# Performance work log

Measured on AMD Instinct MI355X. Metric: run time of the kernel, lower is better.

Reference implementation:

```python
import jax, jax.numpy as jnp
import numpy as np

V, E, G = 25000, 50000, 1024
D_IN, E_IN, D, EH = 74, 12, 64, 128
STEPS, S2S, L, NT = 6, 6, 3, 1


def setup_inputs() -> dict:
    key = jax.random.key(0)
    ks = jax.random.split(key, 20)
    p = lambda k, shp: (jax.random.normal(k, shp, jnp.float32) * 0.05)
    return {
        "node_feats": jax.random.normal(ks[0], (V, D_IN), jnp.float32),
        "edge_feats": jax.random.normal(ks[1], (E, E_IN), jnp.float32),
        "src": jax.random.randint(ks[2], (E,), 0, V),
        "dst": jax.random.randint(ks[3], (E,), 0, V),
        "node2graph": jnp.sort(jax.random.randint(ks[4], (V,), 0, G)),
        "W_proj": p(ks[5], (D_IN, D)), "b_proj": jnp.zeros((D,), jnp.float32),
        "W_e1": p(ks[6], (E_IN, EH)), "b_e1": jnp.zeros((EH,), jnp.float32),
        "W_e2": p(ks[7], (EH, D * D)), "b_e2": jnp.zeros((D * D,), jnp.float32),
        "b_conv": jnp.zeros((D,), jnp.float32),
        "gru_W_ih": p(ks[8], (3 * D, D)), "gru_W_hh": p(ks[9], (3 * D, D)),
        "gru_b_ih": jnp.zeros((3 * D,), jnp.float32), "gru_b_hh": jnp.zeros((3 * D,), jnp.float32),
        "lstm_W_ih0": p(ks[10], (4 * D, 2 * D)), "lstm_W_hh0": p(ks[11], (4 * D, D)),
        "lstm_b_ih0": jnp.zeros((4 * D,), jnp.float32), "lstm_b_hh0": jnp.zeros((4 * D,), jnp.float32),
        "lstm_W_ih_r": p(ks[12], (L - 1, 4 * D, D)), "lstm_W_hh_r": p(ks[13], (L - 1, 4 * D, D)),
        "lstm_b_ih_r": jnp.zeros((L - 1, 4 * D), jnp.float32), "lstm_b_hh_r": jnp.zeros((L - 1, 4 * D), jnp.float32),
        "W1": p(ks[14], (2 * D, D)), "b1": jnp.zeros((D,), jnp.float32),
        "bn_gamma": jnp.ones((D,), jnp.float32), "bn_beta": jnp.zeros((D,), jnp.float32),
        "bn_mean": jnp.zeros((D,), jnp.float32), "bn_var": jnp.ones((D,), jnp.float32),
        "W2": p(ks[15], (D, 4 * NT)), "b2": jnp.zeros((4 * NT,), jnp.float32),
    }


def reference(node_feats, edge_feats, src, dst, node2graph,
              W_proj, b_proj, W_e1, b_e1, W_e2, b_e2, b_conv,
              gru_W_ih, gru_W_hh, gru_b_ih, gru_b_hh,
              lstm_W_ih0, lstm_W_hh0, lstm_b_ih0, lstm_b_hh0,
              lstm_W_ih_r, lstm_W_hh_r, lstm_b_ih_r, lstm_b_hh_r,
              W1, b1, bn_gamma, bn_beta, bn_mean, bn_var, W2, b2):
    # --- MPNNGNN: project + ReLU, then NNConv(sum) + ReLU + GRU, x STEPS ---
    h = jax.nn.relu(node_feats @ W_proj + b_proj)                       # (V, D)
    # edge network: per-edge (D,D) mixing matrix (edge_feats constant across steps)
    We = (jax.nn.relu(edge_feats @ W_e1 + b_e1) @ W_e2 + b_e2).reshape(E, D, D)

    def mp_step(hh, _):
        m = jnp.einsum('ed,edo->eo', hh[src], We)                       # per-edge message
        agg = jax.ops.segment_sum(m, dst, num_segments=V) + b_conv      # NNConv sum + bias
        x = jax.nn.relu(agg)
        gi = x @ gru_W_ih.T + gru_b_ih                                  # GRU (torch gate order r,z,n)
        gh = hh @ gru_W_hh.T + gru_b_hh
        ir, iz, inn = jnp.split(gi, 3, axis=-1)
        hr, hz, hn = jnp.split(gh, 3, axis=-1)
        r = jax.nn.sigmoid(ir + hr)
        z = jax.nn.sigmoid(iz + hz)
        n = jnp.tanh(inn + r * hn)
        return (1.0 - z) * n + z * hh, None

    h, _ = jax.lax.scan(mp_step, h, None, length=STEPS)

    # --- Set2Set readout ---
    q_star = jnp.zeros((G, 2 * D), h.dtype)
    hs = jnp.zeros((L, G, D), h.dtype)
    cs = jnp.zeros((L, G, D), h.dtype)
    for _ in range(S2S):
        x = q_star
        nh, nc = [], []
        for l in range(L):                                              # stacked LSTM, seq len 1
            Wih = lstm_W_ih0 if l == 0 else lstm_W_ih_r[l - 1]
            Whh = lstm_W_hh0 if l == 0 else lstm_W_hh_r[l - 1]
            bih = lstm_b_ih0 if l == 0 else lstm_b_ih_r[l - 1]
            bhh = lstm_b_hh0 if l == 0 else lstm_b_hh_r[l - 1]
            gates = x @ Wih.T + bih + hs[l] @ Whh.T + bhh               # torch order i,f,g,o
            i, f, g, o = jnp.split(gates, 4, axis=-1)
            c = jax.nn.sigmoid(f) * cs[l] + jax.nn.sigmoid(i) * jnp.tanh(g)
            hc = jax.nn.sigmoid(o) * jnp.tanh(c)
            nh.append(hc); nc.append(c)
            x = hc
        hs, cs = jnp.stack(nh), jnp.stack(nc)
        q = x                                                           # (G, D)
        e = jnp.sum(h * q[node2graph], axis=-1)                         # (V,) attention logits
        emax = jax.lax.stop_gradient(jax.ops.segment_max(e, node2graph, num_segments=G))
        emax = jnp.where(jnp.isfinite(emax), emax, 0.0)
        ez = jnp.exp(e - emax[node2graph])                              # per-graph softmax
        denom = jax.ops.segment_sum(ez, node2graph, num_segments=G)
        alpha = ez / jnp.maximum(denom[node2graph], 1e-12)
        readout = jax.ops.segment_sum(h * alpha[:, None], node2graph, num_segments=G)
        q_star = jnp.concatenate([q, readout], axis=-1)                 # (G, 2D)

    # --- evidential head: Linear + ReLU + BatchNorm(eval) + Linear ---
    h1 = jax.nn.relu(q_star @ W1 + b1)
    hbn = bn_gamma * (h1 - bn_mean) * jax.lax.rsqrt(bn_var + 1e-5) + bn_beta
    out = hbn @ W2 + b2                                                 # (G, 4*NT)
    means, logl, loga, logb = jnp.split(out, 4, axis=1)
    MINV = 1e-6
    lam = jax.nn.softplus(logl) + MINV
    alp = jax.nn.softplus(loga) + MINV + 1.0
    bet = jax.nn.softplus(logb) + MINV
    return jnp.stack([means, lam, alp, bet], axis=2).reshape(out.shape)
```

## Files before the change

### kernel.cpp

```cpp
#include <hip/hip_runtime.h>
#include <stdint.h>

#define V_N 25000
#define E_N 50000
#define G_N 1024
#define DIN 74
#define EIN 12
#define NSTEPS 6
#define NS2S 6
#define MPAD 50048

typedef unsigned int u32;
typedef unsigned short u16;
typedef __attribute__((ext_vector_type(8))) short bf16x8v;
typedef __attribute__((ext_vector_type(4))) float f32x4v;

typedef __attribute__((address_space(3))) void lds_void;
typedef __attribute__((address_space(1))) void gbl_void;

__device__ __forceinline__ void gload_lds16(const void* g, void* l) {
  __builtin_amdgcn_global_load_lds((gbl_void*)g, (lds_void*)l, 16, 0, 0);
}

__device__ __forceinline__ u16 f2bf(float f) {
  u32 u = __float_as_uint(f);
  u = (u + 0x7fffu + ((u >> 16) & 1u)) >> 16;
  return (u16)u;
}
__device__ __forceinline__ u32 pack2bf(float lo, float hi) {
  return (u32)f2bf(lo) | ((u32)f2bf(hi) << 16);
}
__device__ __forceinline__ float bflo(u32 w){ return __uint_as_float(w << 16); }
__device__ __forceinline__ float bfhi(u32 w){ return __uint_as_float(w & 0xffff0000u); }
__device__ __forceinline__ float sigf(float x){ return 1.f/(1.f + expf(-x)); }
__device__ __forceinline__ float splusf(float x){ return fmaxf(x, 0.f) + log1pf(expf(-fabsf(x))); }

__global__ void prep_kernel(const float* gWih, const float* gWhh,
                            const float* lWih0, const float* lWhh0,
                            const float* lWihr, const float* lWhhr,
                            const float* We2,
                            float* gWihT, float* gWhhT,
                            u32* TW40, u32* TU40, u32* TW4r, u32* TU4r,
                            u16* WbT) {
  int idx = blockIdx.x * 256 + threadIdx.x;
  if (idx < 12288) { int d = idx / 192, r = idx % 192; gWihT[idx] = gWih[r*64 + d]; return; }
  idx -= 12288;
  if (idx < 12288) { int d = idx / 192, r = idx % 192; gWhhT[idx] = gWhh[r*64 + d]; return; }
  idx -= 12288;
  if (idx < 16384) { int q = idx >> 2, j = idx & 3; int k8 = q >> 8, r = q & 255;
                     TW40[idx] = pack2bf(lWih0[r*128 + k8*8 + 2*j], lWih0[r*128 + k8*8 + 2*j + 1]); return; }
  idx -= 16384;
  if (idx < 8192)  { int q = idx >> 2, j = idx & 3; int k8 = q >> 8, r = q & 255;
                     TU40[idx] = pack2bf(lWhh0[r*64 + k8*8 + 2*j], lWhh0[r*64 + k8*8 + 2*j + 1]); return; }
  idx -= 8192;
  if (idx < 16384) { int l = idx >> 13, rem = idx & 8191; int q = rem >> 2, j = rem & 3;
                     int k8 = q >> 8, r = q & 255;
                     TW4r[idx] = pack2bf(lWihr[l*16384 + r*64 + k8*8 + 2*j],
                                         lWihr[l*16384 + r*64 + k8*8 + 2*j + 1]); return; }
  idx -= 16384;
  if (idx < 16384) { int l = idx >> 13, rem = idx & 8191; int q = rem >> 2, j = rem & 3;
                     int k8 = q >> 8, r = q & 255;
                     TU4r[idx] = pack2bf(lWhhr[l*16384 + r*64 + k8*8 + 2*j],
                                         lWhhr[l*16384 + r*64 + k8*8 + 2*j + 1]); return; }
  idx -= 16384;
  { int n = idx / 128, k = idx % 128; WbT[idx] = f2bf(We2[k*4096 + n]); }
}

__global__ void proj_kernel(const float* nf, const float* Wp, const float* bp, float* h) {
  int v = blockIdx.x * 4 + (threadIdx.x >> 6);
  int o = threadIdx.x & 63;
  if (v >= V_N) return;
  float acc = bp[o];
  const float* row = nf + (size_t)v * DIN;
  #pragma unroll 2
  for (int d = 0; d < DIN; ++d) acc += row[d] * Wp[d*64 + o];
  h[(size_t)v*64 + o] = fmaxf(acc, 0.f);
}

__global__ void edgenet_kernel(const float* ef, const float* W1, const float* b1, u16* zb) {
  int e = blockIdx.x * 2 + (threadIdx.x >> 7);
  int k = threadIdx.x & 127;
  float acc = 0.f;
  if (e < E_N) {
    acc = b1[k];
    const float* row = ef + (size_t)e * EIN;
    #pragma unroll
    for (int i = 0; i < EIN; ++i) acc += row[i] * W1[i*128 + k];
    acc = fmaxf(acc, 0.f);
  }
  zb[(size_t)e*128 + k] = f2bf(acc);
}

__global__ __launch_bounds__(512) void fusedmsg_kernel(const u16* zb, const u16* WbT, const float* be2,
                                                       const float* h, const int* src, const int* dst,
                                                       float* agg) {
  __shared__ __align__(16) u16 Bs[2][8192];
  __shared__ float hS[128][66];
  int t = threadIdx.x;
  int e0 = blockIdx.x * 128;
  int w = t >> 6, lane = t & 63;
  int l16 = lane & 15, lh = lane >> 4;

  for (int it = 0; it < 16; ++it) {
    int idx = it * 512 + t;
    int el = idx >> 6, d = idx & 63;
    int e = e0 + el;
    int sv = (e < E_N) ? src[e] : 0;
    hS[el][d] = h[(size_t)sv * 64 + d];
  }

  bf16x8v af[4];
  #pragma unroll
  for (int ks = 0; ks < 4; ++ks)
    af[ks] = *(const bf16x8v*)(zb + (size_t)(e0 + w*16 + l16)*128 + ks*32 + lh*8);

  {
    const char* Bg = (const char*)WbT;
    char* Bl = (char*)Bs[0];
    #pragma unroll
    for (int it = 0; it < 2; ++it) {
      int f = it * 512 + t;
      int r = f >> 4, s = f & 15;
      int gc = s ^ (r & 7);
      gload_lds16(Bg + r*256 + gc*16, Bl + (size_t)(f & ~63) * 16);
    }
  }
  __syncthreads();

  float macc[4][4];
  #pragma unroll
  for (int of = 0; of < 4; ++of)
    #pragma unroll
    for (int r = 0; r < 4; ++r) macc[of][r] = 0.f;

  for (int d = 0; d < 64; ++d) {
    int buf = d & 1;
    if (d < 63) {
      const char* Bg = (const char*)WbT + (size_t)(d + 1) * 16384;
      char* Bl = (char*)Bs[buf ^ 1];
      #pragma unroll
      for (int it = 0; it < 2; ++it) {
        int f = it * 512 + t;
        int r = f >> 4, s = f & 15;
        int gc = s ^ (r & 7);
        gload_lds16(Bg + r*256 + gc*16, Bl + (size_t)(f & ~63) * 16);
      }
    }
    float hv[4];
    #pragma unroll
    for (int r = 0; r < 4; ++r) hv[r] = hS[w*16 + lh*4 + r][d];

    const char* Bb = (const char*)Bs[buf];
    #pragma unroll
    for (int of = 0; of < 4; ++of) {
      float bias = be2[d*64 + of*16 + l16];
      f32x4v c = (f32x4v){bias, bias, bias, bias};
      #pragma unroll
      for (int ks = 0; ks < 4; ++ks) {
        int brow = of*16 + l16;
        int cb = ks*4 + lh;
        bf16x8v bf = *(const bf16x8v*)(Bb + brow*256 + ((cb ^ (brow & 7)) << 4));
        c = __builtin_amdgcn_mfma_f32_16x16x32_bf16(af[ks], bf, c, 0, 0, 0);
      }
      #pragma unroll
      for (int r = 0; r < 4; ++r) macc[of][r] += hv[r] * c[r];
    }
    __syncthreads();
  }

  #pragma unroll
  for (int r = 0; r < 4; ++r) {
    int row = w*16 + lh*4 + r;
    int e = e0 + row;
    if (e < E_N) {
      int dv = dst[e];
      #pragma unroll
      for (int of = 0; of < 4; ++of)
        atomicAdd(&agg[(size_t)dv*64 + of*16 + l16], macc[of][r]);
    }
  }
}

__global__ void gru_kernel(const float* aggc, const float* bconv, const float* WihT, const float* WhhT,
                           const float* bih, const float* bhh, float* h, float* aggz) {
  int wbase = (blockIdx.x * 4 + (threadIdx.x >> 6)) * 4;
  int o = threadIdx.x & 63;
  float xv[4], hv[4];
  #pragma unroll
  for (int n = 0; n < 4; ++n) {
    int v = wbase + n;
    if (v < V_N) { xv[n] = fmaxf(aggc[(size_t)v*64 + o] + bconv[o], 0.f); hv[n] = h[(size_t)v*64 + o]; }
    else { xv[n] = 0.f; hv[n] = 0.f; }
  }
  float ar[4] = {0,0,0,0}, az[4] = {0,0,0,0}, an[4] = {0,0,0,0};
  float br[4] = {0,0,0,0}, bz[4] = {0,0,0,0}, bn2[4] = {0,0,0,0};
  #pragma unroll 4
  for (int d = 0; d < 64; ++d) {
    float wr = WihT[d*192 + o], wz = WihT[d*192 + 64 + o], wn = WihT[d*192 + 128 + o];
    float ur = WhhT[d*192 + o], uz = WhhT[d*192 + 64 + o], un = WhhT[d*192 + 128 + o];
    #pragma unroll
    for (int n = 0; n < 4; ++n) {
      float xd = __shfl(xv[n], d);
      float hd = __shfl(hv[n], d);
      ar[n] += xd*wr; az[n] += xd*wz; an[n] += xd*wn;
      br[n] += hd*ur; bz[n] += hd*uz; bn2[n] += hd*un;
    }
  }
  float b_r = bih[o] + bhh[o], b_z = bih[64+o] + bhh[64+o];
  float bin = bih[128+o], bhn = bhh[128+o];
  #pragma unroll
  for (int n = 0; n < 4; ++n) {
    int v = wbase + n;
    if (v >= V_N) continue;
    float r  = sigf(ar[n] + br[n] + b_r);
    float z  = sigf(az[n] + bz[n] + b_z);
    float nn = tanhf(an[n] + bin + r*(bn2[n] + bhn));
    h[(size_t)v*64 + o] = (1.f - z)*nn + z*hv[n];
    aggz[(size_t)v*64 + o] = 0.f;
  }
}

__global__ void gstart_kernel(const int* n2g, int* gstart) {
  int g = blockIdx.x * 256 + threadIdx.x;
  if (g > G_N) return;
  int lo = 0, hi = V_N;
  while (lo < hi) { int mid = (lo + hi) >> 1; if (n2g[mid] < g) lo = mid + 1; else hi = mid; }
  gstart[g] = lo;
}

__global__ __launch_bounds__(256) void s2s_kernel(const float* h, const int* gstart,
    const uint4* TW40, const uint4* TU40, const uint4* TW4r, const uint4* TU4r,
    const float* bih0, const float* bhh0, const float* bihr, const float* bhhr,
    float* qstar) {
  __shared__ float sq[4][128];
  __shared__ float sx[4][128];
  __shared__ float shs[4][3][64], scs[4][3][64];
  __shared__ float sg[4][256];
  int tt = threadIdx.x;
  int g0blk = blockIdx.x * 4;
  int w = tt >> 6, lane = tt & 63;
  int nstart = gstart[g0blk + w], nend = gstart[g0blk + w + 1];

  for (int i = tt; i < 512; i += 256) ((float*)sq)[i] = 0.f;
  for (int i = tt; i < 768; i += 256) { ((float*)shs)[i] = 0.f; ((float*)scs)[i] = 0.f; }
  __syncthreads();

  for (int iter = 0; iter < NS2S; ++iter) {
    for (int i = tt; i < 512; i += 256) ((float*)sx)[i] = ((float*)sq)[i];
    __syncthreads();

    for (int l = 0; l < 3; ++l) {
      const uint4* TW = (l == 0) ? TW40 : TW4r + (size_t)(l-1) * 2048;
      const uint4* TU = (l == 0) ? TU40 : TU4r + (size_t)(l-1) * 2048;
      const float* bi = (l == 0) ? bih0 : bihr + (l-1)*256;
      const float* bh = (l == 0) ? bhh0 : bhhr + (l-1)*256;
      float bsum = bi[tt] + bh[tt];
      float acc[4] = {bsum, bsum, bsum, bsum};
      if (l == 0) {
        #pragma unroll
        for (int k8 = 0; k8 < 16; ++k8) {
          uint4 u = TW[k8*256 + tt];
          #pragma unroll
          for (int gi = 0; gi < 4; ++gi) {
            const float4 xa = *(const float4*)&sx[gi][k8*8];
            const float4 xb = *(const float4*)&sx[gi][k8*8 + 4];
            acc[gi] += xa.x*bflo(u.x) + xa.y*bfhi(u.x) + xa.z*bflo(u.y) + xa.w*bfhi(u.y)
                     + xb.x*bflo(u.z) + xb.y*bfhi(u.z) + xb.z*bflo(u.w) + xb.w*bfhi(u.w);
          }
        }
      } else {
        #pragma unroll
        for (int k8 = 0; k8 < 8; ++k8) {
          uint4 u = TW[k8*256 + tt];
          #pragma unroll
          for (int gi = 0; gi < 4; ++gi) {
            const float4 xa = *(const float4*)&sx[gi][k8*8];
            const float4 xb = *(const float4*)&sx[gi][k8*8 + 4];
            acc[gi] += xa.x*bflo(u.x) + xa.y*bfhi(u.x) + xa.z*bflo(u.y) + xa.w*bfhi(u.y)
                     + xb.x*bflo(u.z) + xb.y*bfhi(u.z) + xb.z*bflo(u.w) + xb.w*bfhi(u.w);
          }
        }
      }
      #pragma unroll
      for (int k8 = 0; k8 < 8; ++k8) {
        uint4 u = TU[k8*256 + tt];
        #pragma unroll
        for (int gi = 0; gi < 4; ++gi) {
          const float4 ha = *(const float4*)&shs[gi][l][k8*8];
          const float4 hb = *(const float4*)&shs[gi][l][k8*8 + 4];
          acc[gi] += ha.x*bflo(u.x) + ha.y*bfhi(u.x) + ha.z*bflo(u.y) + ha.w*bfhi(u.y)
                   + hb.x*bflo(u.z) + hb.y*bfhi(u.z) + hb.z*bflo(u.w) + hb.w*bfhi(u.w);
        }
      }
      #pragma unroll
      for (int gi = 0; gi < 4; ++gi) sg[gi][tt] = acc[gi];
      __syncthreads();
      {
        int gq = tt >> 6, r = tt & 63;
        float gv_i = sg[gq][r], gv_f = sg[gq][64+r], gv_g = sg[gq][128+r], gv_o = sg[gq][192+r];
        float c = sigf(gv_f)*scs[gq][l][r] + sigf(gv_i)*tanhf(gv_g);
        float hc = sigf(gv_o)*tanhf(c);
        scs[gq][l][r] = c; shs[gq][l][r] = hc; sx[gq][r] = hc;
      }
      __syncthreads();
    }

    {
      float q_l = sx[w][lane];
      float lmax = -3.4e38f;
      int i = nstart;
      for (; i + 1 < nend; i += 2) {
        float h0 = h[(size_t)i*64 + lane];
        float h1 = h[(size_t)(i+1)*64 + lane];
        float v0 = h0 * q_l, v1 = h1 * q_l;
        #pragma unroll
        for (int off = 32; off; off >>= 1) { v0 += __shfl_xor(v0, off); v1 += __shfl_xor(v1, off); }
        lmax = fmaxf(lmax, fmaxf(v0, v1));
      }
      if (i < nend) {
        float h0 = h[(size_t)i*64 + lane];
        float v0 = h0 * q_l;
        #pragma unroll
        for (int off = 32; off; off >>= 1) v0 += __shfl_xor(v0, off);
        lmax = fmaxf(lmax, v0);
      }
      float lsum = 0.f, accv = 0.f;
      i = nstart;
      for (; i + 1 < nend; i += 2) {
        float h0 = h[(size_t)i*64 + lane];
        float h1 = h[(size_t)(i+1)*64 + lane];
        float v0 = h0 * q_l, v1 = h1 * q_l;
        #pragma unroll
        for (int off = 32; off; off >>= 1) { v0 += __shfl_xor(v0, off); v1 += __shfl_xor(v1, off); }
        float e0 = expf(v0 - lmax), e1 = expf(v1 - lmax);
        lsum += e0 + e1; accv += e0*h0 + e1*h1;
      }
      if (i < nend) {
        float h0 = h[(size_t)i*64 + lane];
        float v0 = h0 * q_l;
        #pragma unroll
        for (int off = 32; off; off >>= 1) v0 += __shfl_xor(v0, off);
        float e0 = expf(v0 - lmax);
        lsum += e0; accv += e0*h0;
      }
      sq[w][lane] = sx[w][lane];
      sq[w][64 + lane] = accv / fmaxf(lsum, 1e-12f);
    }
    __syncthreads();
  }

  for (int i = tt; i < 512; i += 256) qstar[(size_t)g0blk * 128 + i] = ((float*)sq)[i];
}

__global__ void head_kernel(const float* qstar, const float* W1, const float* b1,
                            const float* gma, const float* gbe, const float* gme, const float* gva,
                            const float* W2, const float* b2, float* out) {
  __shared__ float hb[4][64];
  int wslot = threadIdx.x >> 6;
  int g = blockIdx.x * 4 + wslot;
  int o = threadIdx.x & 63;
  float acc = b1[o];
  const float* q = qstar + (size_t)g * 128;
  #pragma unroll 4
  for (int k = 0; k < 128; ++k) acc += q[k] * W1[k*64 + o];
  acc = fmaxf(acc, 0.f);
  float hbn = gma[o] * (acc - gme[o]) * rsqrtf(gva[o] + 1e-5f) + gbe[o];
  hb[wslot][o] = hbn;
  __syncthreads();
  if (o < 4) {
    float v = b2[o];
    #pragma unroll 8
    for (int k = 0; k < 64; ++k) v += hb[wslot][k] * W2[k*4 + o];
    float res;
    if (o == 0) res = v;
    else { res = splusf(v) + 1e-6f; if (o == 2) res += 1.f; }
    out[(size_t)g*4 + o] = res;
  }
}

extern "C" void kernel_launch(void* const* d_in, const int* in_sizes, int n_in,
                              void* d_out, int out_size, void* d_ws, size_t ws_size,
                              hipStream_t stream) {
  const float* node_feats = (const float*)d_in[0];
  const float* edge_feats = (const float*)d_in[1];
  const int*   src        = (const int*)d_in[2];
  const int*   dst        = (const int*)d_in[3];
  const int*   n2g        = (const int*)d_in[4];
  const float* W_proj = (const float*)d_in[5];
  const float* b_proj = (const float*)d_in[6];
  const float* W_e1   = (const float*)d_in[7];
  const float* b_e1   = (const float*)d_in[8];
  const float* W_e2   = (const float*)d_in[9];
  const float* b_e2   = (const float*)d_in[10];
  const float* b_conv = (const float*)d_in[11];
  const float* gru_W_ih = (const float*)d_in[12];
  const float* gru_W_hh = (const float*)d_in[13];
  const float* gru_b_ih = (const float*)d_in[14];
  const float* gru_b_hh = (const float*)d_in[15];
  const float* lstm_W_ih0 = (const float*)d_in[16];
  const float* lstm_W_hh0 = (const float*)d_in[17];
  const float* lstm_b_ih0 = (const float*)d_in[18];
  const float* lstm_b_hh0 = (const float*)d_in[19];
  const float* lstm_W_ih_r = (const float*)d_in[20];
  const float* lstm_W_hh_r = (const float*)d_in[21];
  const float* lstm_b_ih_r = (const float*)d_in[22];
  const float* lstm_b_hh_r = (const float*)d_in[23];
  const float* W1 = (const float*)d_in[24];
  const float* b1 = (const float*)d_in[25];
  const float* bn_gamma = (const float*)d_in[26];
  const float* bn_beta  = (const float*)d_in[27];
  const float* bn_mean  = (const float*)d_in[28];
  const float* bn_var   = (const float*)d_in[29];
  const float* W2 = (const float*)d_in[30];
  const float* b2 = (const float*)d_in[31];

  char* ws = (char*)d_ws;
  size_t off = 0;
  auto alloc = [&](size_t n) { size_t c = off; off += (n + 255) & ~(size_t)255; return c; };
  u16*   zb     = (u16*)  (ws + alloc((size_t)MPAD * 128 * 2));
  float* h      = (float*)(ws + alloc((size_t)V_N * 64 * 4));
  float* agg    = (float*)(ws + alloc((size_t)V_N * 64 * 4));
  u16*   WbT    = (u16*)  (ws + alloc((size_t)4096 * 128 * 2));
  float* gWihT  = (float*)(ws + alloc(12288 * 4));
  float* gWhhT  = (float*)(ws + alloc(12288 * 4));
  u32*   TW40   = (u32*)  (ws + alloc(16384 * 4));
  u32*   TU40   = (u32*)  (ws + alloc(8192 * 4));
  u32*   TW4r   = (u32*)  (ws + alloc(16384 * 4));
  u32*   TU4r   = (u32*)  (ws + alloc(16384 * 4));
  int*   gstart = (int*)  (ws + alloc(1025 * 4));
  float* qstar  = (float*)(ws + alloc((size_t)G_N * 128 * 4));
  (void)in_sizes; (void)n_in; (void)out_size; (void)ws_size;

  prep_kernel<<<2368, 256, 0, stream>>>(gru_W_ih, gru_W_hh, lstm_W_ih0, lstm_W_hh0,
                                        lstm_W_ih_r, lstm_W_hh_r, W_e2,
                                        gWihT, gWhhT, TW40, TU40, TW4r, TU4r, WbT);
  proj_kernel<<<6250, 256, 0, stream>>>(node_feats, W_proj, b_proj, h);
  edgenet_kernel<<<MPAD / 2, 256, 0, stream>>>(edge_feats, W_e1, b_e1, zb);
  hipMemsetAsync(agg, 0, (size_t)V_N * 64 * 4, stream);

  for (int st = 0; st < NSTEPS; ++st) {
    fusedmsg_kernel<<<MPAD / 128, 512, 0, stream>>>(zb, WbT, b_e2, h, src, dst, agg);
    gru_kernel<<<1563, 256, 0, stream>>>(agg, b_conv, gWihT, gWhhT, gru_b_ih, gru_b_hh, h, agg);
  }

  gstart_kernel<<<5, 256, 0, stream>>>(n2g, gstart);
  s2s_kernel<<<256, 256, 0, stream>>>(h, gstart, (const uint4*)TW40, (const uint4*)TU40,
                                      (const uint4*)TW4r, (const uint4*)TU4r,
                                      lstm_b_ih0, lstm_b_hh0, lstm_b_ih_r, lstm_b_hh_r, qstar);
  head_kernel<<<256, 256, 0, stream>>>(qstar, W1, b1, bn_gamma, bn_beta, bn_mean, bn_var,
                                       W2, b2, (float*)d_out);
}
```

Baseline: 1.081 ms.

## Split message kernel over input-dim halves with 2 row fragments per wave

The fused NNConv message kernel now runs two blocks per 128-edge tile, each covering half of the 64 input dimensions, with 256 threads where each wave handles 32 edges (two MFMA row fragments) so every B fragment loaded from LDS feeds two MFMAs. Gathered source features are stored in LDS as bf16 and the edge-net bias slice is staged in LDS. This cuts LDS traffic per MFMA and gives more blocks, at the cost of twice as many atomic adds into agg and reduced precision for the h values. MPAD is raised so the padded edge count is a multiple of 256.

```diff
diff --git a/kernel.cpp b/kernel.cpp
--- a/kernel.cpp
+++ b/kernel.cpp
@@ -8,7 +8,7 @@
 #define EIN 12
 #define NSTEPS 6
 #define NS2S 6
-#define MPAD 50048
+#define MPAD 50176
 
 typedef unsigned int u32;
 typedef unsigned short u16;
@@ -32,6 +32,7 @@
 }
 __device__ __forceinline__ float bflo(u32 w){ return __uint_as_float(w << 16); }
 __device__ __forceinline__ float bfhi(u32 w){ return __uint_as_float(w & 0xffff0000u); }
+__device__ __forceinline__ float bf2f(u16 v){ return __uint_as_float(((u32)v) << 16); }
 __device__ __forceinline__ float sigf(float x){ return 1.f/(1.f + expf(-x)); }
 __device__ __forceinline__ float splusf(float x){ return fmaxf(x, 0.f) + log1pf(expf(-fabsf(x))); }
 
@@ -91,35 +92,43 @@
   zb[(size_t)e*128 + k] = f2bf(acc);
 }
 
-__global__ __launch_bounds__(512) void fusedmsg_kernel(const u16* zb, const u16* WbT, const float* be2,
+__global__ __launch_bounds__(256) void fusedmsg_kernel(const u16* zb, const u16* WbT, const float* be2,
                                                        const float* h, const int* src, const int* dst,
                                                        float* agg) {
   __shared__ __align__(16) u16 Bs[2][8192];
-  __shared__ float hS[128][66];
+  __shared__ u16 hS[128][64];
+  __shared__ float beS[2048];
   int t = threadIdx.x;
-  int e0 = blockIdx.x * 128;
+  int tile = blockIdx.x >> 1, dh = blockIdx.x & 1;
+  int e0 = tile * 128;
+  int d0 = dh * 32;
   int w = t >> 6, lane = t & 63;
   int l16 = lane & 15, lh = lane >> 4;
 
-  for (int it = 0; it < 16; ++it) {
-    int idx = it * 512 + t;
+  #pragma unroll
+  for (int it = 0; it < 8; ++it) beS[it * 256 + t] = be2[d0*64 + it * 256 + t];
+
+  for (int it = 0; it < 32; ++it) {
+    int idx = it * 256 + t;
     int el = idx >> 6, d = idx & 63;
     int e = e0 + el;
     int sv = (e < E_N) ? src[e] : 0;
-    hS[el][d] = h[(size_t)sv * 64 + d];
-  }
-
-  bf16x8v af[4];
-  #pragma unroll
-  for (int ks = 0; ks < 4; ++ks)
-    af[ks] = *(const bf16x8v*)(zb + (size_t)(e0 + w*16 + l16)*128 + ks*32 + lh*8);
+    hS[el][d] = f2bf(h[(size_t)sv * 64 + d]);
+  }
+
+  bf16x8v af[2][4];
+  #pragma unroll
+  for (int rf = 0; rf < 2; ++rf)
+    #pragma unroll
+    for (int ks = 0; ks < 4; ++ks)
+      af[rf][ks] = *(const bf16x8v*)(zb + (size_t)(e0 + w*32 + rf*16 + l16)*128 + ks*32 + lh*8);
 
   {
-    const char* Bg = (const char*)WbT;
+    const char* Bg = (const char*)(WbT + (size_t)d0 * 8192);
     char* Bl = (char*)Bs[0];
     #pragma unroll
-    for (int it = 0; it < 2; ++it) {
-      int f = it * 512 + t;
+    for (int it = 0; it < 4; ++it) {
+      int f = it * 256 + t;
       int r = f >> 4, s = f & 15;
       int gc = s ^ (r & 7);
       gload_lds16(Bg + r*256 + gc*16, Bl + (size_t)(f & ~63) * 16);
@@ -127,58 +136,71 @@
   }
   __syncthreads();
 
-  float macc[4][4];
-  #pragma unroll
-  for (int of = 0; of < 4; ++of)
-    #pragma unroll
-    for (int r = 0; r < 4; ++r) macc[of][r] = 0.f;
-
-  for (int d = 0; d < 64; ++d) {
-    int buf = d & 1;
-    if (d < 63) {
-      const char* Bg = (const char*)WbT + (size_t)(d + 1) * 16384;
+  float macc[2][4][4];
+  #pragma unroll
+  for (int rf = 0; rf < 2; ++rf)
+    #pragma unroll
+    for (int of = 0; of < 4; ++of)
+      #pragma unroll
+      for (int r = 0; r < 4; ++r) macc[rf][of][r] = 0.f;
+
+  for (int nt = 0; nt < 32; ++nt) {
+    int d = d0 + nt;
+    int buf = nt & 1;
+    if (nt < 31) {
+      const char* Bg = (const char*)(WbT + (size_t)(d + 1) * 8192);
       char* Bl = (char*)Bs[buf ^ 1];
       #pragma unroll
-      for (int it = 0; it < 2; ++it) {
-        int f = it * 512 + t;
+      for (int it = 0; it < 4; ++it) {
+        int f = it * 256 + t;
         int r = f >> 4, s = f & 15;
         int gc = s ^ (r & 7);
         gload_lds16(Bg + r*256 + gc*16, Bl + (size_t)(f & ~63) * 16);
       }
     }
-    float hv[4];
-    #pragma unroll
-    for (int r = 0; r < 4; ++r) hv[r] = hS[w*16 + lh*4 + r][d];
+    float hv[2][4];
+    #pragma unroll
+    for (int rf = 0; rf < 2; ++rf)
+      #pragma unroll
+      for (int r = 0; r < 4; ++r)
+        hv[rf][r] = bf2f(hS[w*32 + rf*16 + lh*4 + r][d]);
 
     const char* Bb = (const char*)Bs[buf];
     #pragma unroll
     for (int of = 0; of < 4; ++of) {
-      float bias = be2[d*64 + of*16 + l16];
-      f32x4v c = (f32x4v){bias, bias, bias, bias};
+      float bias = beS[nt*64 + of*16 + l16];
+      f32x4v c0 = (f32x4v){bias, bias, bias, bias};
+      f32x4v c1 = c0;
       #pragma unroll
       for (int ks = 0; ks < 4; ++ks) {
         int brow = of*16 + l16;
         int cb = ks*4 + lh;
         bf16x8v bf = *(const bf16x8v*)(Bb + brow*256 + ((cb ^ (brow & 7)) << 4));
-        c = __builtin_amdgcn_mfma_f32_16x16x32_bf16(af[ks], bf, c, 0, 0, 0);
-      }
-      #pragma unroll
-      for (int r = 0; r < 4; ++r) macc[of][r] += hv[r] * c[r];
+        c0 = __builtin_amdgcn_mfma_f32_16x16x32_bf16(af[0][ks], bf, c0, 0, 0, 0);
+        c1 = __builtin_amdgcn_mfma_f32_16x16x32_bf16(af[1][ks], bf, c1, 0, 0, 0);
+      }
+      #pragma unroll
+      for (int r = 0; r < 4; ++r) {
+        macc[0][of][r] += hv[0][r] * c0[r];
+        macc[1][of][r] += hv[1][r] * c1[r];
+      }
     }
     __syncthreads();
   }
 
   #pragma unroll
-  for (int r = 0; r < 4; ++r) {
-    int row = w*16 + lh*4 + r;
-    int e = e0 + row;
-    if (e < E_N) {
-      int dv = dst[e];
-      #pragma unroll
-      for (int of = 0; of < 4; ++of)
-        atomicAdd(&agg[(size_t)dv*64 + of*16 + l16], macc[of][r]);
-    }
-  }
+  for (int rf = 0; rf < 2; ++rf)
+    #pragma unroll
+    for (int r = 0; r < 4; ++r) {
+      int row = w*32 + rf*16 + lh*4 + r;
+      int e = e0 + row;
+      if (e < E_N) {
+        int dv = dst[e];
+        #pragma unroll
+        for (int of = 0; of < 4; ++of)
+          atomicAdd(&agg[(size_t)dv*64 + of*16 + l16], macc[rf][of][r]);
+      }
+    }
 }
 
 __global__ void gru_kernel(const float* aggc, const float* bconv, const float* WihT, const float* WhhT,
@@ -439,7 +461,7 @@
   hipMemsetAsync(agg, 0, (size_t)V_N * 64 * 4, stream);
 
   for (int st = 0; st < NSTEPS; ++st) {
-    fusedmsg_kernel<<<MPAD / 128, 512, 0, stream>>>(zb, WbT, b_e2, h, src, dst, agg);
+    fusedmsg_kernel<<<(MPAD / 128) * 2, 256, 0, stream>>>(zb, WbT, b_e2, h, src, dst, agg);
     gru_kernel<<<1563, 256, 0, stream>>>(agg, b_conv, gWihT, gWhhT, gru_b_ih, gru_b_hh, h, agg);
   }
 
```

Measured after the change: 1.283 ms. +18.7%, slower.

## Triple-buffer edge-weight tiles, cache bias and bf16 h in LDS, widen GRU

Applied to the files above, without the earlier changes.

The fused message kernel moves from double to triple buffering of the per-d weight tiles. Its full __syncthreads is replaced by explicit vmcnt waits and a raw barrier, so loads run two iterations ahead. The e2 bias is staged in LDS, and gathered source features are stored as bf16 to save LDS, which adds rounding error to h. The GRU kernel processes 8 nodes per wave instead of 4 to reuse weight loads, at higher register pressure. MPAD also changes.

```diff
diff --git a/kernel.cpp b/kernel.cpp
--- a/kernel.cpp
+++ b/kernel.cpp
@@ -8,7 +8,7 @@
 #define EIN 12
 #define NSTEPS 6
 #define NS2S 6
-#define MPAD 50048
+#define MPAD 50176
 
 typedef unsigned int u32;
 typedef unsigned short u16;
@@ -32,6 +32,7 @@
 }
 __device__ __forceinline__ float bflo(u32 w){ return __uint_as_float(w << 16); }
 __device__ __forceinline__ float bfhi(u32 w){ return __uint_as_float(w & 0xffff0000u); }
+__device__ __forceinline__ float bf2f(u16 v){ return __uint_as_float(((u32)v) << 16); }
 __device__ __forceinline__ float sigf(float x){ return 1.f/(1.f + expf(-x)); }
 __device__ __forceinline__ float splusf(float x){ return fmaxf(x, 0.f) + log1pf(expf(-fabsf(x))); }
 
@@ -94,19 +95,23 @@
 __global__ __launch_bounds__(512) void fusedmsg_kernel(const u16* zb, const u16* WbT, const float* be2,
                                                        const float* h, const int* src, const int* dst,
                                                        float* agg) {
-  __shared__ __align__(16) u16 Bs[2][8192];
-  __shared__ float hS[128][66];
+  __shared__ __align__(16) u16 Bs[3][8192];
+  __shared__ u16 hS[128][64];
+  __shared__ float beS[4096];
   int t = threadIdx.x;
   int e0 = blockIdx.x * 128;
   int w = t >> 6, lane = t & 63;
   int l16 = lane & 15, lh = lane >> 4;
 
+  #pragma unroll
+  for (int it = 0; it < 8; ++it) beS[it * 512 + t] = be2[it * 512 + t];
+
   for (int it = 0; it < 16; ++it) {
     int idx = it * 512 + t;
-    int el = idx >> 6, d = idx & 63;
+    int el = idx >> 6, dd = idx & 63;
     int e = e0 + el;
     int sv = (e < E_N) ? src[e] : 0;
-    hS[el][d] = h[(size_t)sv * 64 + d];
+    hS[el][dd] = f2bf(h[(size_t)sv * 64 + dd]);
   }
 
   bf16x8v af[4];
@@ -114,9 +119,10 @@
   for (int ks = 0; ks < 4; ++ks)
     af[ks] = *(const bf16x8v*)(zb + (size_t)(e0 + w*16 + l16)*128 + ks*32 + lh*8);
 
-  {
-    const char* Bg = (const char*)WbT;
-    char* Bl = (char*)Bs[0];
+  #pragma unroll
+  for (int pd = 0; pd < 2; ++pd) {
+    const char* Bg = (const char*)(WbT + (size_t)pd * 8192);
+    char* Bl = (char*)Bs[pd];
     #pragma unroll
     for (int it = 0; it < 2; ++it) {
       int f = it * 512 + t;
@@ -134,10 +140,9 @@
     for (int r = 0; r < 4; ++r) macc[of][r] = 0.f;
 
   for (int d = 0; d < 64; ++d) {
-    int buf = d & 1;
-    if (d < 63) {
-      const char* Bg = (const char*)WbT + (size_t)(d + 1) * 16384;
-      char* Bl = (char*)Bs[buf ^ 1];
+    if (d < 62) {
+      const char* Bg = (const char*)(WbT + (size_t)(d + 2) * 8192);
+      char* Bl = (char*)Bs[(d + 2) % 3];
       #pragma unroll
       for (int it = 0; it < 2; ++it) {
         int f = it * 512 + t;
@@ -145,15 +150,22 @@
         int gc = s ^ (r & 7);
         gload_lds16(Bg + r*256 + gc*16, Bl + (size_t)(f & ~63) * 16);
       }
-    }
+      asm volatile("s_waitcnt vmcnt(4)" ::: "memory");
+    } else if (d == 62) {
+      asm volatile("s_waitcnt vmcnt(2)" ::: "memory");
+    } else {
+      asm volatile("s_waitcnt vmcnt(0)" ::: "memory");
+    }
+    __builtin_amdgcn_s_barrier();
+
     float hv[4];
     #pragma unroll
-    for (int r = 0; r < 4; ++r) hv[r] = hS[w*16 + lh*4 + r][d];
-
-    const char* Bb = (const char*)Bs[buf];
+    for (int r = 0; r < 4; ++r) hv[r] = bf2f(hS[w*16 + lh*4 + r][d]);
+
+    const char* Bb = (const char*)Bs[d % 3];
     #pragma unroll
     for (int of = 0; of < 4; ++of) {
-      float bias = be2[d*64 + of*16 + l16];
+      float bias = beS[d*64 + of*16 + l16];
       f32x4v c = (f32x4v){bias, bias, bias, bias};
       #pragma unroll
       for (int ks = 0; ks < 4; ++ks) {
@@ -165,7 +177,8 @@
       #pragma unroll
       for (int r = 0; r < 4; ++r) macc[of][r] += hv[r] * c[r];
     }
-    __syncthreads();
+    asm volatile("s_waitcnt lgkmcnt(0)" ::: "memory");
+    __builtin_amdgcn_s_barrier();
   }
 
   #pragma unroll
@@ -183,23 +196,23 @@
 
 __global__ void gru_kernel(const float* aggc, const float* bconv, const float* WihT, const float* WhhT,
                            const float* bih, const float* bhh, float* h, float* aggz) {
-  int wbase = (blockIdx.x * 4 + (threadIdx.x >> 6)) * 4;
+  int wbase = (blockIdx.x * 4 + (threadIdx.x >> 6)) * 8;
   int o = threadIdx.x & 63;
-  float xv[4], hv[4];
-  #pragma unroll
-  for (int n = 0; n < 4; ++n) {
+  float xv[8], hv[8];
+  #pragma unroll
+  for (int n = 0; n < 8; ++n) {
     int v = wbase + n;
     if (v < V_N) { xv[n] = fmaxf(aggc[(size_t)v*64 + o] + bconv[o], 0.f); hv[n] = h[(size_t)v*64 + o]; }
     else { xv[n] = 0.f; hv[n] = 0.f; }
   }
-  float ar[4] = {0,0,0,0}, az[4] = {0,0,0,0}, an[4] = {0,0,0,0};
-  float br[4] = {0,0,0,0}, bz[4] = {0,0,0,0}, bn2[4] = {0,0,0,0};
+  float ar[8] = {0,0,0,0,0,0,0,0}, az[8] = {0,0,0,0,0,0,0,0}, an[8] = {0,0,0,0,0,0,0,0};
+  float br[8] = {0,0,0,0,0,0,0,0}, bz[8] = {0,0,0,0,0,0,0,0}, bn2[8] = {0,0,0,0,0,0,0,0};
   #pragma unroll 4
   for (int d = 0; d < 64; ++d) {
     float wr = WihT[d*192 + o], wz = WihT[d*192 + 64 + o], wn = WihT[d*192 + 128 + o];
     float ur = WhhT[d*192 + o], uz = WhhT[d*192 + 64 + o], un = WhhT[d*192 + 128 + o];
     #pragma unroll
-    for (int n = 0; n < 4; ++n) {
+    for (int n = 0; n < 8; ++n) {
       float xd = __shfl(xv[n], d);
       float hd = __shfl(hv[n], d);
       ar[n] += xd*wr; az[n] += xd*wz; an[n] += xd*wn;
@@ -209,7 +222,7 @@
   float b_r = bih[o] + bhh[o], b_z = bih[64+o] + bhh[64+o];
   float bin = bih[128+o], bhn = bhh[128+o];
   #pragma unroll
-  for (int n = 0; n < 4; ++n) {
+  for (int n = 0; n < 8; ++n) {
     int v = wbase + n;
     if (v >= V_N) continue;
     float r  = sigf(ar[n] + br[n] + b_r);
@@ -440,7 +453,7 @@
 
   for (int st = 0; st < NSTEPS; ++st) {
     fusedmsg_kernel<<<MPAD / 128, 512, 0, stream>>>(zb, WbT, b_e2, h, src, dst, agg);
-    gru_kernel<<<1563, 256, 0, stream>>>(agg, b_conv, gWihT, gWhhT, gru_b_ih, gru_b_hh, h, agg);
+    gru_kernel<<<782, 256, 0, stream>>>(agg, b_conv, gWihT, gWhhT, gru_b_ih, gru_b_hh, h, agg);
   }
 
   gstart_kernel<<<5, 256, 0, stream>>>(n2g, gstart);
```

Result: slower. 1.155 ms (+6.8%).
